# Kernel optimization log

Hardware: AMD Instinct MI355X
Metric: run time of the kernel (lower is better)

Reference implementation:

```python
import jax, jax.numpy as jnp
import numpy as np

B, T, DIM = 2, 2048, 1024
H, HD = 16, 64          # num_heads, head_dim (DIM = H*HD)
SCALE = 0.12            # fixed attn_scale in the module
ROPE_BASE = 1024.0
EPS = 1e-6


def _rope_tables(seq_len, head_dim):
    half = head_dim // 2
    keep = head_dim // 4
    active = (1.0 / ROPE_BASE) ** jnp.linspace(0.0, 1.0, keep, dtype=jnp.float32)
    inv_freq = jnp.concatenate([active, jnp.zeros(half - keep, dtype=jnp.float32)])
    theta = jnp.arange(seq_len, dtype=jnp.float32)[:, None] * inv_freq[None, :]  # [T, half]
    return jnp.cos(theta), jnp.sin(theta)


def _rms_norm(x):
    # F.rms_norm without learned scale
    return x * jax.lax.rsqrt(jnp.mean(x * x, axis=-1, keepdims=True) + EPS)


def _apply_rope(x_bthd, cos, sin):
    # x_bthd: [B,T,H,HD]; cos/sin: [T, HD/2]
    xf = x_bthd.astype(jnp.float32)
    x1, x2 = jnp.split(xf, 2, axis=-1)
    c = cos[None, :, None, :]
    s = sin[None, :, None, :]
    y = jnp.concatenate([x1 * c + x2 * s, -x1 * s + x2 * c], axis=-1)
    return y.astype(x_bthd.dtype)


def setup_inputs() -> dict:
    key = jax.random.key(0)
    k1, k2, k3, k4 = jax.random.split(key, 4)
    x = jax.random.normal(k1, (B, T, DIM), dtype=jnp.float32)
    ve = jax.random.normal(k2, (B, T, DIM), dtype=jnp.float32)
    sa_lambdas = jax.random.uniform(k3, (2,), dtype=jnp.float32)
    # additive causal mask, as SDPA receives a float mask cast to q dtype
    causal = jnp.tril(jnp.ones((T, T), dtype=bool))
    attn_mask = jnp.where(causal, 0.0, -1e9).astype(jnp.float32)[None, None]
    # qkvo weights; scaled like a typical linear init (original zero-inits W_o,
    # here kept random so the output is non-trivial for kernel testing)
    qkvo_w = jax.random.normal(k4, (4, DIM, DIM), dtype=jnp.float32) * (DIM ** -0.5)
    return {"x": x, "ve": ve, "sa_lambdas": sa_lambdas, "attn_mask": attn_mask, "qkvo_w": qkvo_w}


def reference(x, ve, sa_lambdas, attn_mask, qkvo_w):
    b, t, _ = x.shape
    # fused QKV projection: qkvo_w[:3] is [3, DIM, DIM], F.linear -> x @ W.T
    qkv = jnp.einsum('btd,ked->btke', x, qkvo_w[:3])          # [B,T,3,DIM]
    q = _rms_norm(qkv[:, :, 0].reshape(b, t, H, HD))
    k = _rms_norm(qkv[:, :, 1].reshape(b, t, H, HD))
    v = _rms_norm(qkv[:, :, 2].reshape(b, t, H, HD))
    cos, sin = _rope_tables(t, HD)
    q = _apply_rope(q, cos, sin)
    k = _apply_rope(k, cos, sin)
    # value-embedding blend
    v = sa_lambdas[0] * v + sa_lambdas[1] * ve.reshape(b, t, H, HD)
    # attention with fixed scale and additive mask
    scores = jnp.einsum('bthd,bshd->bhts', q, k) * SCALE + attn_mask
    att = jax.nn.softmax(scores, axis=-1)
    y = jnp.einsum('bhts,bshd->bthd', att, v).reshape(b, t, DIM)
    return y @ qkvo_w[3].T
```

## Files before the change

### kernel.cpp

```cpp
#include <hip/hip_runtime.h>
#include <hip/hip_bf16.h>
#include <stdint.h>

#define T_SEQ 2048
#define DIMSZ 1024
#define NH    16
#define HDIM  64
#define NBATCH 2
#define KVB   64
#define ATT_SCALE 0.12f
#define QSCALE (0.12f * 1.4426950408889634f)

typedef __attribute__((ext_vector_type(8))) __bf16 bf16x8;
typedef __attribute__((ext_vector_type(8))) ushort u16x8;
typedef __attribute__((ext_vector_type(4))) float f32x4;

#define GLOAD_LDS16(gp, lp)                                                            \
  __builtin_amdgcn_global_load_lds((const __attribute__((address_space(1))) void*)(gp),\
                                   (__attribute__((address_space(3))) void*)(lp),      \
                                   16, 0, 0)

__device__ __forceinline__ ushort f2bf(float f) {
  union { float f; uint32_t u; } v; v.f = f;
  uint32_t u = v.u;
  uint32_t r = (u + 0x7FFFu + ((u >> 16) & 1u)) >> 16;
  return (ushort)r;
}

__device__ __forceinline__ float bf2f(ushort h) {
  union { float f; uint32_t u; } v;
  v.u = ((uint32_t)h) << 16;
  return v.f;
}

__device__ __forceinline__ uint32_t pk2(float a, float b) {
  union { __hip_bfloat162 h; uint32_t u; } cv;
  cv.h = __hip_bfloat162(__float2bfloat16(a), __float2bfloat16(b));
  return cv.u;
}

__global__ __launch_bounds__(256) void prep_k(const float* __restrict__ x,
                                              const float* __restrict__ w,
                                              ushort* __restrict__ Xb,
                                              ushort* __restrict__ Wb,
                                              float* __restrict__ ctab,
                                              float* __restrict__ stab) {
  int bid = blockIdx.x;
  int tid = threadIdx.x;
  if (bid < 4096) {
    int i = (bid * 256 + tid) * 4;
    float4 v = *(const float4*)(x + i);
    ushort4 o;
    o.x = f2bf(v.x); o.y = f2bf(v.y); o.z = f2bf(v.z); o.w = f2bf(v.w);
    *(ushort4*)(Xb + i) = o;
  } else if (bid < 8192) {
    int i = ((bid - 4096) * 256 + tid) * 4;
    float4 v = *(const float4*)(w + i);
    ushort4 o;
    o.x = f2bf(v.x); o.y = f2bf(v.y); o.z = f2bf(v.z); o.w = f2bf(v.w);
    *(ushort4*)(Wb + i) = o;
  } else {
    int idx = (bid - 8192) * 256 + tid;
    int j = idx & 31, t = idx >> 5;
    float c = 1.f, s = 0.f;
    if (j < 16) {
      float inv = powf(1024.0f, -(float)j / 15.0f);
      float th = (float)t * inv;
      c = cosf(th);
      s = sinf(th);
    }
    ctab[idx] = c;
    stab[idx] = s;
  }
}

#define BM 128
#define BN 128
#define BKS 64

__global__ __launch_bounds__(256) void gemm_qkv_k(const ushort* __restrict__ A,
                                                  const ushort* __restrict__ Bt,
                                                  const float* __restrict__ ve,
                                                  const float* __restrict__ lam,
                                                  const float* __restrict__ ctab,
                                                  const float* __restrict__ stab,
                                                  ushort* __restrict__ Qb,
                                                  ushort* __restrict__ Kb,
                                                  ushort* __restrict__ Vt) {
  const int K = DIMSZ;
  __shared__ __align__(16) ushort As[BM * BKS];
  __shared__ __align__(16) ushort Bs[BN * BKS];
  int tid = threadIdx.x;
  int wave = tid >> 6, lane = tid & 63;
  int lr = lane & 15, lg = lane >> 4;
  int m0 = blockIdx.x * BM, n0 = blockIdx.y * BN;
  int wm = (wave >> 1) * 64, wn = (wave & 1) * 64;

  int srow = tid >> 3;
  int sel = (((tid & 7) ^ (srow & 7)) << 3);

  f32x4 acc[4][4];
  for (int m = 0; m < 4; ++m)
    for (int n = 0; n < 4; ++n)
      acc[m][n] = (f32x4){0.f, 0.f, 0.f, 0.f};

  for (int k0 = 0; k0 < K; k0 += BKS) {
#pragma unroll
    for (int it = 0; it < 4; ++it) {
      GLOAD_LDS16(A + (size_t)(m0 + it * 32 + srow) * K + k0 + sel, &As[(it * 256 + tid) * 8]);
      GLOAD_LDS16(Bt + (size_t)(n0 + it * 32 + srow) * K + k0 + sel, &Bs[(it * 256 + tid) * 8]);
    }
    __syncthreads();
#pragma unroll
    for (int kk = 0; kk < 2; ++kk) {
      int cA = (((kk * 4 + lg) ^ (lr & 7)) << 3);
      bf16x8 af[4], bf[4];
#pragma unroll
      for (int m = 0; m < 4; ++m)
        af[m] = *(const bf16x8*)&As[(wm + m * 16 + lr) * BKS + cA];
#pragma unroll
      for (int n = 0; n < 4; ++n)
        bf[n] = *(const bf16x8*)&Bs[(wn + n * 16 + lr) * BKS + cA];
#pragma unroll
      for (int m = 0; m < 4; ++m)
#pragma unroll
        for (int n = 0; n < 4; ++n)
          acc[m][n] = __builtin_amdgcn_mfma_f32_16x16x32_bf16(af[m], bf[n], acc[m][n], 0, 0, 0);
    }
    __syncthreads();
  }

  int sec = n0 >> 10;
  int h = ((n0 & 1023) + wn) >> 6;
  ushort* Tl = (wave < 2 ? As : Bs) + (wave & 1) * 4096;

#pragma unroll
  for (int m = 0; m < 4; ++m)
#pragma unroll
    for (int n = 0; n < 4; ++n)
#pragma unroll
      for (int r = 0; r < 4; ++r) {
        int tl = m * 16 + lg * 4 + r;
        int d = n * 16 + lr;
        Tl[tl * 64 + ((((d >> 3) ^ (tl & 7)) << 3) | (d & 7))] = f2bf(acc[m][n][r]);
      }

  int tl = lane;
  float xv[64];
#pragma unroll
  for (int j = 0; j < 8; ++j) {
    u16x8 rw = *(const u16x8*)&Tl[tl * 64 + ((j ^ (tl & 7)) << 3)];
#pragma unroll
    for (int e = 0; e < 8; ++e) xv[j * 8 + e] = bf2f((ushort)rw[e]);
  }

  float ss = 0.f;
#pragma unroll
  for (int i = 0; i < 64; ++i) ss += xv[i] * xv[i];
  float rinv = rsqrtf(ss * (1.0f / 64.0f) + 1e-6f);
#pragma unroll
  for (int i = 0; i < 64; ++i) xv[i] *= rinv;

  int row = m0 + wm + tl;
  int t = row & (T_SEQ - 1);
  int bb = row >> 11;
  int bh = bb * NH + h;

  if (sec < 2) {
    float cs[16], sn[16];
    const float4* cp = (const float4*)(ctab + t * 32);
    const float4* sp = (const float4*)(stab + t * 32);
#pragma unroll
    for (int j = 0; j < 4; ++j) {
      float4 c4 = cp[j], s4 = sp[j];
      cs[j * 4 + 0] = c4.x; cs[j * 4 + 1] = c4.y; cs[j * 4 + 2] = c4.z; cs[j * 4 + 3] = c4.w;
      sn[j * 4 + 0] = s4.x; sn[j * 4 + 1] = s4.y; sn[j * 4 + 2] = s4.z; sn[j * 4 + 3] = s4.w;
    }
#pragma unroll
    for (int j = 0; j < 16; ++j) {
      float a = xv[j], bv = xv[j + 32];
      xv[j] = a * cs[j] + bv * sn[j];
      xv[j + 32] = bv * cs[j] - a * sn[j];
    }
    float sc = (sec == 0) ? QSCALE : 1.0f;
    ushort* dst = (sec == 0 ? Qb : Kb) + ((size_t)bh * T_SEQ + t) * HDIM;
#pragma unroll
    for (int p = 0; p < 8; ++p) {
      uint4 wq = make_uint4(pk2(xv[8 * p] * sc, xv[8 * p + 1] * sc),
                            pk2(xv[8 * p + 2] * sc, xv[8 * p + 3] * sc),
                            pk2(xv[8 * p + 4] * sc, xv[8 * p + 5] * sc),
                            pk2(xv[8 * p + 6] * sc, xv[8 * p + 7] * sc));
      *((uint4*)dst + p) = wq;
    }
  } else {
    float l0 = lam[0], l1 = lam[1];
    const float4* vp = (const float4*)(ve + ((size_t)(bb * T_SEQ + t)) * DIMSZ + h * HDIM);
#pragma unroll
    for (int j = 0; j < 16; ++j) {
      float4 vv4 = vp[j];
      xv[j * 4 + 0] = l0 * xv[j * 4 + 0] + l1 * vv4.x;
      xv[j * 4 + 1] = l0 * xv[j * 4 + 1] + l1 * vv4.y;
      xv[j * 4 + 2] = l0 * xv[j * 4 + 2] + l1 * vv4.z;
      xv[j * 4 + 3] = l0 * xv[j * 4 + 3] + l1 * vv4.w;
    }
    ushort* dst = Vt + (size_t)bh * HDIM * T_SEQ + t;
#pragma unroll
    for (int i = 0; i < 64; ++i)
      dst[(size_t)i * T_SEQ] = f2bf(xv[i]);
  }
}

__global__ __launch_bounds__(256) void gemm_out_k(const ushort* __restrict__ A,
                                                  const ushort* __restrict__ Bt,
                                                  float* __restrict__ C) {
  const int K = DIMSZ, N = DIMSZ;
  __shared__ __align__(16) ushort As[64 * BKS];
  __shared__ __align__(16) ushort Bs[128 * BKS];
  int tid = threadIdx.x;
  int wave = tid >> 6, lane = tid & 63;
  int lr = lane & 15, lg = lane >> 4;
  int m0 = blockIdx.x * 64, n0 = blockIdx.y * 128;
  int wm = (wave >> 1) * 32, wn = (wave & 1) * 64;

  int srow = tid >> 3;
  int sel = (((tid & 7) ^ (srow & 7)) << 3);

  f32x4 acc[2][4];
#pragma unroll
  for (int m = 0; m < 2; ++m)
#pragma unroll
    for (int n = 0; n < 4; ++n)
      acc[m][n] = (f32x4){0.f, 0.f, 0.f, 0.f};

  for (int k0 = 0; k0 < K; k0 += BKS) {
#pragma unroll
    for (int it = 0; it < 2; ++it)
      GLOAD_LDS16(A + (size_t)(m0 + it * 32 + srow) * K + k0 + sel, &As[(it * 256 + tid) * 8]);
#pragma unroll
    for (int it = 0; it < 4; ++it)
      GLOAD_LDS16(Bt + (size_t)(n0 + it * 32 + srow) * K + k0 + sel, &Bs[(it * 256 + tid) * 8]);
    __syncthreads();
#pragma unroll
    for (int kk = 0; kk < 2; ++kk) {
      int cA = (((kk * 4 + lg) ^ (lr & 7)) << 3);
      bf16x8 af[2], bf[4];
#pragma unroll
      for (int m = 0; m < 2; ++m)
        af[m] = *(const bf16x8*)&As[(wm + m * 16 + lr) * BKS + cA];
#pragma unroll
      for (int n = 0; n < 4; ++n)
        bf[n] = *(const bf16x8*)&Bs[(wn + n * 16 + lr) * BKS + cA];
#pragma unroll
      for (int m = 0; m < 2; ++m)
#pragma unroll
        for (int n = 0; n < 4; ++n)
          acc[m][n] = __builtin_amdgcn_mfma_f32_16x16x32_bf16(af[m], bf[n], acc[m][n], 0, 0, 0);
    }
    __syncthreads();
  }
#pragma unroll
  for (int m = 0; m < 2; ++m)
#pragma unroll
    for (int n = 0; n < 4; ++n)
#pragma unroll
      for (int r = 0; r < 4; ++r) {
        int row = m0 + wm + m * 16 + lg * 4 + r;
        int col = n0 + wn + n * 16 + lr;
        C[(size_t)row * N + col] = acc[m][n][r];
      }
}

__global__ __launch_bounds__(256, 3) void attn_k(const ushort* __restrict__ Q,
                                                 const ushort* __restrict__ K,
                                                 const ushort* __restrict__ Vt,
                                                 ushort* __restrict__ Y) {
  int bh = blockIdx.x;
  int qb = 31 - blockIdx.y;
  int tid = threadIdx.x;
  int wid = tid >> 6, lane = tid & 63;
  int lr = lane & 15, lg = lane >> 4;
  int b = bh >> 4, h = bh & 15;

  int r0 = qb * 64 + wid * 16;
  int nkv = qb + 1;

  __shared__ __align__(16) ushort Kl[2][KVB * HDIM];
  __shared__ __align__(16) ushort Vl[2][KVB * HDIM];
  __shared__ __align__(16) ushort Plds[4][16][72];

  const ushort* Kbh = K + (size_t)bh * T_SEQ * HDIM;
  const ushort* Vbh = Vt + (size_t)bh * HDIM * T_SEQ;

  int sr = tid >> 3;
  int sel = (((tid & 7) ^ (sr & 7)) << 3);
  const ushort* ksrc0 = Kbh + (size_t)sr * HDIM + sel;
  const ushort* ksrc1 = Kbh + (size_t)(sr + 32) * HDIM + sel;
  const ushort* vsrc0 = Vbh + (size_t)sr * T_SEQ + sel;
  const ushort* vsrc1 = Vbh + (size_t)(sr + 32) * T_SEQ + sel;
  int ld0 = tid * 8, ld1 = tid * 8 + 2048;

  const ushort* Qbase = Q + ((size_t)bh * T_SEQ + r0) * HDIM;
  bf16x8 aq[2];
#pragma unroll
  for (int kk = 0; kk < 2; ++kk)
    aq[kk] = *(const bf16x8*)(Qbase + (size_t)lr * HDIM + kk * 32 + lg * 8);

  int fcol[2];
  fcol[0] = ((0 + lg) ^ (lr & 7)) << 3;
  fcol[1] = ((4 + lg) ^ (lr & 7)) << 3;

  f32x4 o[4];
#pragma unroll
  for (int n = 0; n < 4; ++n) o[n] = (f32x4){0.f, 0.f, 0.f, 0.f};
  float lrow = 0.f;

  GLOAD_LDS16(ksrc0, &Kl[0][ld0]);
  GLOAD_LDS16(ksrc1, &Kl[0][ld1]);
  GLOAD_LDS16(vsrc0, &Vl[0][ld0]);
  GLOAD_LDS16(vsrc1, &Vl[0][ld1]);
  __syncthreads();

  for (int kb = 0; kb < nkv; ++kb) {
    int cur = kb & 1;
    if (kb + 1 < nkv) {
      size_t ko = (size_t)(kb + 1) * KVB * HDIM;
      int vo = (kb + 1) * KVB;
      GLOAD_LDS16(ksrc0 + ko, &Kl[cur ^ 1][ld0]);
      GLOAD_LDS16(ksrc1 + ko, &Kl[cur ^ 1][ld1]);
      GLOAD_LDS16(vsrc0 + vo, &Vl[cur ^ 1][ld0]);
      GLOAD_LDS16(vsrc1 + vo, &Vl[cur ^ 1][ld1]);
    }
    const ushort* Kc = &Kl[cur][0];
    const ushort* Vc = &Vl[cur][0];
    f32x4 s[4];
    __builtin_amdgcn_s_setprio(1);
#pragma unroll
    for (int n = 0; n < 4; ++n) {
      f32x4 a = (f32x4){0.f, 0.f, 0.f, 0.f};
      bf16x8 kf0 = *(const bf16x8*)&Kc[(n * 16 + lr) * HDIM + fcol[0]];
      a = __builtin_amdgcn_mfma_f32_16x16x32_bf16(kf0, aq[0], a, 0, 0, 0);
      bf16x8 kf1 = *(const bf16x8*)&Kc[(n * 16 + lr) * HDIM + fcol[1]];
      a = __builtin_amdgcn_mfma_f32_16x16x32_bf16(kf1, aq[1], a, 0, 0, 0);
      s[n] = a;
    }
    __builtin_amdgcn_s_setprio(0);
    if (kb == nkv - 1) {
      int qrow = r0 + lr;
      int kb0 = kb * KVB + lg * 4;
#pragma unroll
      for (int n = 0; n < 4; ++n)
#pragma unroll
        for (int r = 0; r < 4; ++r)
          if (kb0 + n * 16 + r > qrow) s[n][r] = -1e30f;
    }
    float psum = 0.f;
#pragma unroll
    for (int n = 0; n < 4; ++n) {
      float p0 = exp2f(s[n][0]), p1 = exp2f(s[n][1]);
      float p2 = exp2f(s[n][2]), p3 = exp2f(s[n][3]);
      psum += (p0 + p1) + (p2 + p3);
      uint2 w;
      w.x = pk2(p0, p1);
      w.y = pk2(p2, p3);
      *(uint2*)&Plds[wid][lr][n * 16 + lg * 4] = w;
    }
    lrow += psum;
    __builtin_amdgcn_s_setprio(1);
#pragma unroll
    for (int kk = 0; kk < 2; ++kk) {
      bf16x8 ap = *(const bf16x8*)&Plds[wid][lr][kk * 32 + lg * 8];
#pragma unroll
      for (int n = 0; n < 4; ++n) {
        bf16x8 vf = *(const bf16x8*)&Vc[(n * 16 + lr) * HDIM + fcol[kk]];
        o[n] = __builtin_amdgcn_mfma_f32_16x16x32_bf16(vf, ap, o[n], 0, 0, 0);
      }
    }
    __builtin_amdgcn_s_setprio(0);
    __syncthreads();
  }
  lrow += __shfl_xor(lrow, 16);
  lrow += __shfl_xor(lrow, 32);
  float inv = 1.0f / lrow;
  int row = r0 + lr;
#pragma unroll
  for (int n = 0; n < 4; ++n) {
    uint2 w;
    w.x = pk2(o[n][0] * inv, o[n][1] * inv);
    w.y = pk2(o[n][2] * inv, o[n][3] * inv);
    *(uint2*)&Y[((size_t)b * T_SEQ + row) * DIMSZ + h * HDIM + n * 16 + lg * 4] = w;
  }
}

extern "C" void kernel_launch(void* const* d_in, const int* in_sizes, int n_in,
                              void* d_out, int out_size, void* d_ws, size_t ws_size,
                              hipStream_t stream) {
  const float* x   = (const float*)d_in[0];
  const float* ve  = (const float*)d_in[1];
  const float* lam = (const float*)d_in[2];
  const float* w   = (const float*)d_in[4];
  float* out = (float*)d_out;

  char* ws = (char*)d_ws;

  ushort* Xb   = (ushort*)(ws);
  ushort* Wb   = (ushort*)(ws + 8388608);
  ushort* Qb   = (ushort*)(ws + 16777216);
  ushort* Kb   = (ushort*)(ws + 25165824);
  ushort* Vt   = (ushort*)(ws + 33554432);
  ushort* Yb   = (ushort*)(ws + 41943040);
  float*  ctab = (float*)(ws + 50331648);
  float*  stab = (float*)(ws + 50593792);

  prep_k<<<8448, 256, 0, stream>>>(x, w, Xb, Wb, ctab, stab);

  gemm_qkv_k<<<dim3(4096 / BM, 3072 / BN), 256, 0, stream>>>(Xb, Wb, ve, lam, ctab, stab,
                                                             Qb, Kb, Vt);

  attn_k<<<dim3(NBATCH * NH, 32), 256, 0, stream>>>(Qb, Kb, Vt, Yb);

  gemm_out_k<<<dim3(4096 / 64, 1024 / 128), 256, 0, stream>>>(Yb, Wb + 3ull * DIMSZ * DIMSZ, out);
}
```

Before: 117.8 us.

## Switch attention to 32x32x16 MFMA with two 32-row waves per block

Rewrites the attention kernel to use 32x32x16 bf16 MFMA tiles instead of 16x16x32. Each block now has 2 waves covering 32 query rows each, so a block is 128 threads instead of 256, and the K/V staging loop is adjusted to match. The P tile in LDS switches to an XOR-swizzled layout. The larger MFMA tiles read fewer LDS fragments per FLOP, at the cost of fewer waves per block, higher register use and a changed causal-masking index map.

```diff
diff --git a/kernel.cpp b/kernel.cpp
--- a/kernel.cpp
+++ b/kernel.cpp
@@ -14,6 +14,7 @@
 typedef __attribute__((ext_vector_type(8))) __bf16 bf16x8;
 typedef __attribute__((ext_vector_type(8))) ushort u16x8;
 typedef __attribute__((ext_vector_type(4))) float f32x4;
+typedef __attribute__((ext_vector_type(16))) float f32x16;
 
 #define GLOAD_LDS16(gp, lp)                                                            \
   __builtin_amdgcn_global_load_lds((const __attribute__((address_space(1))) void*)(gp),\
@@ -270,54 +271,48 @@
       }
 }
 
-__global__ __launch_bounds__(256, 3) void attn_k(const ushort* __restrict__ Q,
-                                                 const ushort* __restrict__ K,
-                                                 const ushort* __restrict__ Vt,
-                                                 ushort* __restrict__ Y) {
+__global__ __launch_bounds__(128) void attn_k(const ushort* __restrict__ Q,
+                                              const ushort* __restrict__ K,
+                                              const ushort* __restrict__ Vt,
+                                              ushort* __restrict__ Y) {
   int bh = blockIdx.x;
   int qb = 31 - blockIdx.y;
   int tid = threadIdx.x;
   int wid = tid >> 6, lane = tid & 63;
-  int lr = lane & 15, lg = lane >> 4;
+  int l5 = lane >> 5;
+  int q = lane & 31;
   int b = bh >> 4, h = bh & 15;
 
-  int r0 = qb * 64 + wid * 16;
+  int r0 = qb * 64 + wid * 32;
   int nkv = qb + 1;
 
   __shared__ __align__(16) ushort Kl[2][KVB * HDIM];
   __shared__ __align__(16) ushort Vl[2][KVB * HDIM];
-  __shared__ __align__(16) ushort Plds[4][16][72];
+  __shared__ __align__(16) ushort Plds[2][32][64];
 
   const ushort* Kbh = K + (size_t)bh * T_SEQ * HDIM;
   const ushort* Vbh = Vt + (size_t)bh * HDIM * T_SEQ;
 
   int sr = tid >> 3;
   int sel = (((tid & 7) ^ (sr & 7)) << 3);
-  const ushort* ksrc0 = Kbh + (size_t)sr * HDIM + sel;
-  const ushort* ksrc1 = Kbh + (size_t)(sr + 32) * HDIM + sel;
-  const ushort* vsrc0 = Vbh + (size_t)sr * T_SEQ + sel;
-  const ushort* vsrc1 = Vbh + (size_t)(sr + 32) * T_SEQ + sel;
-  int ld0 = tid * 8, ld1 = tid * 8 + 2048;
-
-  const ushort* Qbase = Q + ((size_t)bh * T_SEQ + r0) * HDIM;
-  bf16x8 aq[2];
-#pragma unroll
-  for (int kk = 0; kk < 2; ++kk)
-    aq[kk] = *(const bf16x8*)(Qbase + (size_t)lr * HDIM + kk * 32 + lg * 8);
-
-  int fcol[2];
-  fcol[0] = ((0 + lg) ^ (lr & 7)) << 3;
-  fcol[1] = ((4 + lg) ^ (lr & 7)) << 3;
-
-  f32x4 o[4];
-#pragma unroll
-  for (int n = 0; n < 4; ++n) o[n] = (f32x4){0.f, 0.f, 0.f, 0.f};
+  const ushort* ksrc = Kbh + (size_t)sr * HDIM + sel;
+  const ushort* vsrc = Vbh + (size_t)sr * T_SEQ + sel;
+  int ldb = tid * 8;
+
+  const ushort* Qrow = Q + ((size_t)bh * T_SEQ + r0 + q) * HDIM;
+  bf16x8 bq[4];
+#pragma unroll
+  for (int s = 0; s < 4; ++s)
+    bq[s] = *(const bf16x8*)(Qrow + s * 16 + l5 * 8);
+
+  f32x16 o0 = {0}, o1 = {0};
   float lrow = 0.f;
 
-  GLOAD_LDS16(ksrc0, &Kl[0][ld0]);
-  GLOAD_LDS16(ksrc1, &Kl[0][ld1]);
-  GLOAD_LDS16(vsrc0, &Vl[0][ld0]);
-  GLOAD_LDS16(vsrc1, &Vl[0][ld1]);
+#pragma unroll
+  for (int j = 0; j < 4; ++j) {
+    GLOAD_LDS16(ksrc + (size_t)j * 16 * HDIM, &Kl[0][ldb + j * 1024]);
+    GLOAD_LDS16(vsrc + (size_t)j * 16 * T_SEQ, &Vl[0][ldb + j * 1024]);
+  }
   __syncthreads();
 
   for (int kb = 0; kb < nkv; ++kb) {
@@ -325,70 +320,90 @@
     if (kb + 1 < nkv) {
       size_t ko = (size_t)(kb + 1) * KVB * HDIM;
       int vo = (kb + 1) * KVB;
-      GLOAD_LDS16(ksrc0 + ko, &Kl[cur ^ 1][ld0]);
-      GLOAD_LDS16(ksrc1 + ko, &Kl[cur ^ 1][ld1]);
-      GLOAD_LDS16(vsrc0 + vo, &Vl[cur ^ 1][ld0]);
-      GLOAD_LDS16(vsrc1 + vo, &Vl[cur ^ 1][ld1]);
+#pragma unroll
+      for (int j = 0; j < 4; ++j) {
+        GLOAD_LDS16(ksrc + ko + (size_t)j * 16 * HDIM, &Kl[cur ^ 1][ldb + j * 1024]);
+        GLOAD_LDS16(vsrc + vo + (size_t)j * 16 * T_SEQ, &Vl[cur ^ 1][ldb + j * 1024]);
+      }
     }
     const ushort* Kc = &Kl[cur][0];
     const ushort* Vc = &Vl[cur][0];
-    f32x4 s[4];
+
+    f32x16 s0 = {0}, s1 = {0};
     __builtin_amdgcn_s_setprio(1);
 #pragma unroll
-    for (int n = 0; n < 4; ++n) {
-      f32x4 a = (f32x4){0.f, 0.f, 0.f, 0.f};
-      bf16x8 kf0 = *(const bf16x8*)&Kc[(n * 16 + lr) * HDIM + fcol[0]];
-      a = __builtin_amdgcn_mfma_f32_16x16x32_bf16(kf0, aq[0], a, 0, 0, 0);
-      bf16x8 kf1 = *(const bf16x8*)&Kc[(n * 16 + lr) * HDIM + fcol[1]];
-      a = __builtin_amdgcn_mfma_f32_16x16x32_bf16(kf1, aq[1], a, 0, 0, 0);
-      s[n] = a;
+    for (int s = 0; s < 4; ++s) {
+      int cA = (((s * 2 + l5) ^ (q & 7)) << 3);
+      bf16x8 kf0 = *(const bf16x8*)&Kc[(0 * 32 + q) * 64 + cA];
+      s0 = __builtin_amdgcn_mfma_f32_32x32x16_bf16(kf0, bq[s], s0, 0, 0, 0);
+      bf16x8 kf1 = *(const bf16x8*)&Kc[(1 * 32 + q) * 64 + cA];
+      s1 = __builtin_amdgcn_mfma_f32_32x32x16_bf16(kf1, bq[s], s1, 0, 0, 0);
     }
     __builtin_amdgcn_s_setprio(0);
+
     if (kb == nkv - 1) {
-      int qrow = r0 + lr;
-      int kb0 = kb * KVB + lg * 4;
-#pragma unroll
-      for (int n = 0; n < 4; ++n)
-#pragma unroll
-        for (int r = 0; r < 4; ++r)
-          if (kb0 + n * 16 + r > qrow) s[n][r] = -1e30f;
+      int qrow = r0 + q;
+      int kb0 = kb * KVB + 4 * l5;
+#pragma unroll
+      for (int reg = 0; reg < 16; ++reg) {
+        int kidx = kb0 + (reg & 3) + 8 * (reg >> 2);
+        if (kidx > qrow) s0[reg] = -1e30f;
+        if (kidx + 32 > qrow) s1[reg] = -1e30f;
+      }
     }
     float psum = 0.f;
 #pragma unroll
-    for (int n = 0; n < 4; ++n) {
-      float p0 = exp2f(s[n][0]), p1 = exp2f(s[n][1]);
-      float p2 = exp2f(s[n][2]), p3 = exp2f(s[n][3]);
-      psum += (p0 + p1) + (p2 + p3);
-      uint2 w;
-      w.x = pk2(p0, p1);
-      w.y = pk2(p2, p3);
-      *(uint2*)&Plds[wid][lr][n * 16 + lg * 4] = w;
+    for (int hh = 0; hh < 2; ++hh) {
+#pragma unroll
+      for (int g = 0; g < 4; ++g) {
+        float p0, p1, p2, p3;
+        if (hh == 0) {
+          p0 = exp2f(s0[4 * g + 0]); p1 = exp2f(s0[4 * g + 1]);
+          p2 = exp2f(s0[4 * g + 2]); p3 = exp2f(s0[4 * g + 3]);
+        } else {
+          p0 = exp2f(s1[4 * g + 0]); p1 = exp2f(s1[4 * g + 1]);
+          p2 = exp2f(s1[4 * g + 2]); p3 = exp2f(s1[4 * g + 3]);
+        }
+        psum += (p0 + p1) + (p2 + p3);
+        uint2 w;
+        w.x = pk2(p0, p1);
+        w.y = pk2(p2, p3);
+        *(uint2*)&Plds[wid][q][(((g + 4 * hh) ^ (q & 7)) << 3) + 4 * l5] = w;
+      }
     }
     lrow += psum;
     __builtin_amdgcn_s_setprio(1);
 #pragma unroll
-    for (int kk = 0; kk < 2; ++kk) {
-      bf16x8 ap = *(const bf16x8*)&Plds[wid][lr][kk * 32 + lg * 8];
-#pragma unroll
-      for (int n = 0; n < 4; ++n) {
-        bf16x8 vf = *(const bf16x8*)&Vc[(n * 16 + lr) * HDIM + fcol[kk]];
-        o[n] = __builtin_amdgcn_mfma_f32_16x16x32_bf16(vf, ap, o[n], 0, 0, 0);
-      }
+    for (int s = 0; s < 4; ++s) {
+      bf16x8 bp = *(const bf16x8*)&Plds[wid][q][((s * 2 + l5) ^ (q & 7)) << 3];
+      int cV = (((s * 2 + l5) ^ (q & 7)) << 3);
+      bf16x8 vf0 = *(const bf16x8*)&Vc[(0 * 32 + q) * 64 + cV];
+      o0 = __builtin_amdgcn_mfma_f32_32x32x16_bf16(vf0, bp, o0, 0, 0, 0);
+      bf16x8 vf1 = *(const bf16x8*)&Vc[(1 * 32 + q) * 64 + cV];
+      o1 = __builtin_amdgcn_mfma_f32_32x32x16_bf16(vf1, bp, o1, 0, 0, 0);
     }
     __builtin_amdgcn_s_setprio(0);
     __syncthreads();
   }
-  lrow += __shfl_xor(lrow, 16);
   lrow += __shfl_xor(lrow, 32);
   float inv = 1.0f / lrow;
-  int row = r0 + lr;
-#pragma unroll
-  for (int n = 0; n < 4; ++n) {
-    uint2 w;
-    w.x = pk2(o[n][0] * inv, o[n][1] * inv);
-    w.y = pk2(o[n][2] * inv, o[n][3] * inv);
-    *(uint2*)&Y[((size_t)b * T_SEQ + row) * DIMSZ + h * HDIM + n * 16 + lg * 4] = w;
-  }
+  int row = r0 + q;
+  ushort* dst = Y + ((size_t)b * T_SEQ + row) * DIMSZ + h * HDIM;
+#pragma unroll
+  for (int db = 0; db < 2; ++db)
+#pragma unroll
+    for (int g = 0; g < 4; ++g) {
+      float v0, v1, v2, v3;
+      if (db == 0) {
+        v0 = o0[4 * g + 0]; v1 = o0[4 * g + 1]; v2 = o0[4 * g + 2]; v3 = o0[4 * g + 3];
+      } else {
+        v0 = o1[4 * g + 0]; v1 = o1[4 * g + 1]; v2 = o1[4 * g + 2]; v3 = o1[4 * g + 3];
+      }
+      uint2 w;
+      w.x = pk2(v0 * inv, v1 * inv);
+      w.y = pk2(v2 * inv, v3 * inv);
+      *(uint2*)&dst[8 * g + 4 * l5 + 32 * db] = w;
+    }
 }
 
 extern "C" void kernel_launch(void* const* d_in, const int* in_sizes, int n_in,
@@ -416,7 +431,7 @@
   gemm_qkv_k<<<dim3(4096 / BM, 3072 / BN), 256, 0, stream>>>(Xb, Wb, ve, lam, ctab, stab,
                                                              Qb, Kb, Vt);
 
-  attn_k<<<dim3(NBATCH * NH, 32), 256, 0, stream>>>(Qb, Kb, Vt, Yb);
+  attn_k<<<dim3(NBATCH * NH, 32), 128, 0, stream>>>(Qb, Kb, Vt, Yb);
 
   gemm_out_k<<<dim3(4096 / 64, 1024 / 128), 256, 0, stream>>>(Yb, Wb + 3ull * DIMSZ * DIMSZ, out);
 }
```

After: 137.3 us. 1.17x slower.
